# Performance work log

Hardware: AMD Instinct MI355X
Metric: run time of the kernel (lower is better)

The kernel has to match this reference:

```python
import jax, jax.numpy as jnp
import numpy as np

N = 100000   # num nodes
E = 2000000  # num edges
D = 32       # feature dim (input_dim == hidden)
L = 6        # num layers
R = 50       # num relations
B = 64       # num query source nodes
EPS = 1e-6


def setup_inputs() -> dict:
    key = jax.random.key(0)
    ks = jax.random.split(key, 7)
    edge_index = jax.random.randint(ks[0], (E, 2), 0, N)
    edge_type = jax.random.randint(ks[1], (E,), 0, R)
    edge_weight = jnp.ones((E,), jnp.float32)
    h_index = jax.random.randint(ks[2], (B,), 0, N)
    rel_emb = jax.random.normal(ks[3], (L, R, D), jnp.float32) * 0.1
    W = jax.random.normal(ks[4], (L, 13 * D, D), jnp.float32) * (1.0 / np.sqrt(13 * D))
    b = jnp.zeros((L, D), jnp.float32)
    return dict(edge_index=edge_index, edge_type=edge_type, edge_weight=edge_weight,
                h_index=h_index, rel_emb=rel_emb, W=W, b=b)


def _layer(x, boundary, node_in, node_out, edge_type, edge_weight, rel, W, b, degree_out):
    # message: distmult  (E, D)
    msg = x[node_in] * rel[edge_type]
    # append boundary as self-loop messages -> (E+N, D)
    msg = jnp.concatenate([msg, boundary], axis=0)
    seg = jnp.concatenate([node_out, jnp.arange(N)], axis=0)
    w = jnp.concatenate([edge_weight, jnp.ones((N,), x.dtype)], axis=0)[:, None]
    mw = msg * w
    cnt = jax.ops.segment_sum(jnp.ones_like(w), seg, num_segments=N)  # (N,1), >=1
    mean = jax.ops.segment_sum(mw, seg, num_segments=N) / cnt
    sq_mean = jax.ops.segment_sum((msg * msg) * w, seg, num_segments=N) / cnt
    mx = jax.ops.segment_max(mw, seg, num_segments=N)
    mn = jax.ops.segment_min(mw, seg, num_segments=N)
    std = jnp.sqrt(jnp.clip(sq_mean - mean * mean, EPS, None))
    # interleave per-channel [mean, max, min, std] -> (N, 4D)
    feat = jnp.stack([mean, mx, mn, std], axis=-1).reshape(N, 4 * D)
    scale = jnp.log(degree_out)              # (N, 1)
    scale = scale / scale.mean()
    scales = jnp.concatenate([jnp.ones_like(scale), scale,
                              1.0 / jnp.clip(scale, 1e-2, None)], axis=-1)  # (N, 3)
    update = (feat[:, :, None] * scales[:, None, :]).reshape(N, 12 * D)
    out = jnp.concatenate([x, update], axis=-1) @ W + b  # (N, D)
    return jax.nn.relu(out)


def reference(edge_index, edge_type, edge_weight, h_index, rel_emb, W, b):
    node_in = edge_index[:, 0]
    node_out = edge_index[:, 1]
    boundary = jnp.zeros((N, D), jnp.float32).at[h_index].set(1.0)
    degree_out = (jax.ops.segment_sum(edge_weight, node_out, num_segments=N) + 1.0)[:, None]
    x = boundary
    for i in range(L):
        x = _layer(x, boundary, node_in, node_out, edge_type, edge_weight,
                   rel_emb[i], W[i], b[i], degree_out)
    return x  # node_feature (N, D)
```

## Files before the change

### kernel.cpp

```cpp
#include <hip/hip_runtime.h>
#include <math.h>

#define NN 100000
#define EE 2000000
#define DD 32
#define LL 6
#define RR 50
#define BB 64
#define SCAN_BLK 98


typedef __attribute__((ext_vector_type(8))) short bf16x8;
typedef __attribute__((ext_vector_type(4))) float f32x4;

__device__ __forceinline__ unsigned short f2bf(float f) {
    unsigned int u = __float_as_uint(f);
    u = (u + 0x7FFFu + ((u >> 16) & 1u)) >> 16;
    return (unsigned short)u;
}
__device__ __forceinline__ float bf2f(unsigned short h) {
    return __uint_as_float((unsigned int)h << 16);
}

__global__ void hist_kernel(const int* __restrict__ ei, int* __restrict__ cnt) {
    for (int e = blockIdx.x * blockDim.x + threadIdx.x; e < EE; e += gridDim.x * blockDim.x)
        atomicAdd(&cnt[ei[2 * e + 1]], 1);
}

__global__ void boundary_kernel(const int* __restrict__ h, float* __restrict__ bnd,
                                float* __restrict__ x0, unsigned short* __restrict__ xbf0) {
    int t = blockIdx.x * blockDim.x + threadIdx.x;
    if (t >= BB * DD) return;
    int bidx = t >> 5, d = t & 31;
    int node = h[bidx];
    x0[node * DD + d] = 1.0f;
    if (xbf0) xbf0[node * DD + d] = 0x3F80;
    if (d == 0) bnd[node] = 1.0f;
}

__global__ void scanA_kernel(const int* __restrict__ cnt, int* __restrict__ rowptr,
                             int* __restrict__ bsum) {
    __shared__ int sh[1024];
    const int idx = blockIdx.x * 1024 + threadIdx.x;
    const int v = (idx < NN) ? cnt[idx] : 0;
    sh[threadIdx.x] = v;
    __syncthreads();
    for (int off = 1; off < 1024; off <<= 1) {
        int t = (threadIdx.x >= (unsigned)off) ? sh[threadIdx.x - off] : 0;
        __syncthreads();
        sh[threadIdx.x] += t;
        __syncthreads();
    }
    if (idx < NN) rowptr[idx] = sh[threadIdx.x] - v;
    if (threadIdx.x == 1023) bsum[blockIdx.x] = sh[1023];
}

__global__ void scanB_kernel(const int* __restrict__ bsum, int* __restrict__ boff,
                             int* __restrict__ rowptr) {
    __shared__ int sh[128];
    const int t = threadIdx.x;
    const int v = (t < SCAN_BLK) ? bsum[t] : 0;
    sh[t] = v;
    __syncthreads();
    for (int off = 1; off < 128; off <<= 1) {
        int u = (t >= off) ? sh[t - off] : 0;
        __syncthreads();
        sh[t] += u;
        __syncthreads();
    }
    if (t < SCAN_BLK) boff[t] = sh[t] - v;
    if (t == SCAN_BLK - 1) rowptr[NN] = sh[t];
}

__global__ void scanC_kernel(int* __restrict__ rowptr, int* __restrict__ cursor,
                             const int* __restrict__ boff) {
    const int idx = blockIdx.x * 1024 + threadIdx.x;
    if (idx < NN) {
        const int r = rowptr[idx] + boff[blockIdx.x];
        rowptr[idx] = r;
        cursor[idx] = r;
    }
}

__global__ void logsum_kernel(const int* __restrict__ cnt, double* __restrict__ out) {
    __shared__ double sh[256];
    double local = 0.0;
    for (int i = blockIdx.x * blockDim.x + threadIdx.x; i < NN; i += gridDim.x * blockDim.x)
        local += log((double)cnt[i] + 1.0);
    sh[threadIdx.x] = local;
    __syncthreads();
    for (int o = 128; o > 0; o >>= 1) {
        if (threadIdx.x < (unsigned)o) sh[threadIdx.x] += sh[threadIdx.x + o];
        __syncthreads();
    }
    if (threadIdx.x == 0) atomicAdd(out, sh[0]);
}

__global__ void scalefin_kernel(const int* __restrict__ cnt, const double* __restrict__ logsum,
                                float* __restrict__ scalev, float* __restrict__ iscalev) {
    float mean = (float)(logsum[0] / (double)NN);
    for (int i = blockIdx.x * blockDim.x + threadIdx.x; i < NN; i += gridDim.x * blockDim.x) {
        float s = logf((float)cnt[i] + 1.0f) / mean;
        scalev[i] = s;
        iscalev[i] = 1.0f / fmaxf(s, 0.01f);
    }
}

__global__ void scatterX_kernel(const int* __restrict__ ei, const int* __restrict__ et,
                                int* __restrict__ cursor, int* __restrict__ recs) {
    const int slice = blockIdx.x & 7;
    const int sb = blockIdx.x >> 3;
    const int nsb = gridDim.x >> 3;
    const int lo = slice * (NN / 8);
    const int hi = (slice == 7) ? NN : lo + (NN / 8);
    const int2* ei2 = (const int2*)ei;
    for (int e = sb * blockDim.x + threadIdx.x; e < EE; e += nsb * blockDim.x) {
        const int2 p = ei2[e];
        if (p.y >= lo && p.y < hi) {
            const int pos = atomicAdd(&cursor[p.y], 1);
            recs[pos] = (p.x << 6) | et[e];
        }
    }
}

__global__ __launch_bounds__(256, 4) void aggbf_kernel(
    const unsigned short* __restrict__ xbf, float* __restrict__ feat,
    const int* __restrict__ recs, const int* __restrict__ rowptr,
    const float* __restrict__ bnd, const float* __restrict__ rel_l) {
    __shared__ float rel_s[RR * 32];
    {
        const float4* r4 = (const float4*)rel_l;
        float4* rs4 = (float4*)rel_s;
        for (int i = threadIdx.x; i < (RR * 32) / 4; i += 256) rs4[i] = r4[i];
    }
    __syncthreads();

    const int lane = threadIdx.x & 63;
    const int half = lane >> 5;
    const int d = lane & 31;
    const int wid = blockIdx.x * 4 + (threadIdx.x >> 6);
    const int nwaves = gridDim.x * 4;

    for (int n0 = wid * 2; n0 < NN; n0 += nwaves * 2) {
        const int nA = n0, nB = n0 + 1;
        const int rowA = rowptr[nA], endA = rowptr[nA + 1];
        const int rowB = rowptr[nB], endB = rowptr[nB + 1];
        const float bvA = bnd[nA], bvB = bnd[nB];

        float sA = (half == 0) ? bvA : 0.f, qA = sA;
        float mxA = bvA, mnA = bvA;
        float sB = (half == 0) ? bvB : 0.f, qB = sB;
        float mxB = bvB, mnB = bvB;

        int eA = rowA + half, eB = rowB + half;

#define ACC_A(M) { sA += (M); qA = fmaf((M), (M), qA); mxA = fmaxf(mxA, (M)); mnA = fminf(mnA, (M)); }
#define ACC_B(M) { sB += (M); qB = fmaf((M), (M), qB); mxB = fmaxf(mxB, (M)); mnB = fminf(mnB, (M)); }
#define MSG(P) (bf2f(xbf[((P) >> 6) * DD + d]) * rel_s[((P) & 63) * DD + d])

        while (eA + 6 < endA && eB + 6 < endB) {
            const int pa0 = recs[eA], pa1 = recs[eA + 2], pa2 = recs[eA + 4], pa3 = recs[eA + 6];
            const int pb0 = recs[eB], pb1 = recs[eB + 2], pb2 = recs[eB + 4], pb3 = recs[eB + 6];
            const float ma0 = MSG(pa0), ma1 = MSG(pa1), ma2 = MSG(pa2), ma3 = MSG(pa3);
            const float mb0 = MSG(pb0), mb1 = MSG(pb1), mb2 = MSG(pb2), mb3 = MSG(pb3);
            ACC_A(ma0); ACC_A(ma1); ACC_A(ma2); ACC_A(ma3);
            ACC_B(mb0); ACC_B(mb1); ACC_B(mb2); ACC_B(mb3);
            eA += 8; eB += 8;
        }
        while (eA + 2 < endA) {
            const int pa0 = recs[eA], pa1 = recs[eA + 2];
            const float ma0 = MSG(pa0), ma1 = MSG(pa1);
            ACC_A(ma0); ACC_A(ma1);
            eA += 4;
        }
        while (eB + 2 < endB) {
            const int pb0 = recs[eB], pb1 = recs[eB + 2];
            const float mb0 = MSG(pb0), mb1 = MSG(pb1);
            ACC_B(mb0); ACC_B(mb1);
            eB += 4;
        }
        if (eA < endA) { const float m0 = MSG(recs[eA]); ACC_A(m0); }
        if (eB < endB) { const float m0 = MSG(recs[eB]); ACC_B(m0); }
#undef MSG
#undef ACC_A
#undef ACC_B

        sA += __shfl_xor(sA, 32); qA += __shfl_xor(qA, 32);
        mxA = fmaxf(mxA, __shfl_xor(mxA, 32)); mnA = fminf(mnA, __shfl_xor(mnA, 32));
        sB += __shfl_xor(sB, 32); qB += __shfl_xor(qB, 32);
        mxB = fmaxf(mxB, __shfl_xor(mxB, 32)); mnB = fminf(mnB, __shfl_xor(mnB, 32));

        const float invA = 1.0f / (float)(endA - rowA + 1);
        const float invB = 1.0f / (float)(endB - rowB + 1);
        if (half == 0) {
            const float mean = sA * invA;
            const float stdv = sqrtf(fmaxf(qA * invA - mean * mean, 1e-6f));
            float* fb = feat + (size_t)nA * 128;
            fb[d] = mean; fb[32 + d] = mxA; fb[64 + d] = mnA; fb[96 + d] = stdv;
        } else {
            const float mean = sB * invB;
            const float stdv = sqrtf(fmaxf(qB * invB - mean * mean, 1e-6f));
            float* fb = feat + (size_t)nB * 128;
            fb[d] = mean; fb[32 + d] = mxB; fb[64 + d] = mnB; fb[96 + d] = stdv;
        }
    }
}

__global__ __launch_bounds__(256, 4) void agg_kernel(
    const float* __restrict__ xin, float* __restrict__ feat,
    const int* __restrict__ recs, const int* __restrict__ rowptr,
    const float* __restrict__ bnd, const float* __restrict__ rel_l) {
    __shared__ float rel_s[RR * 32];
    {
        const float4* r4 = (const float4*)rel_l;
        float4* rs4 = (float4*)rel_s;
        for (int i = threadIdx.x; i < (RR * 32) / 4; i += 256) rs4[i] = r4[i];
    }
    __syncthreads();

    const int lane = threadIdx.x & 63;
    const int half = lane >> 5;
    const int d = lane & 31;
    const int wid = blockIdx.x * 4 + (threadIdx.x >> 6);
    const int nwaves = gridDim.x * 4;

    for (int n0 = wid * 2; n0 < NN; n0 += nwaves * 2) {
        const int nA = n0, nB = n0 + 1;
        const int rowA = rowptr[nA], endA = rowptr[nA + 1];
        const int rowB = rowptr[nB], endB = rowptr[nB + 1];
        const float bvA = bnd[nA], bvB = bnd[nB];

        float sA = (half == 0) ? bvA : 0.f, qA = sA;
        float mxA = bvA, mnA = bvA;
        float sB = (half == 0) ? bvB : 0.f, qB = sB;
        float mxB = bvB, mnB = bvB;

        int eA = rowA + half, eB = rowB + half;
#define STEP_A { const int p0_ = recs[eA]; const int p1_ = recs[eA + 2];                  \
        const float m0_ = xin[(p0_ >> 6) * DD + d] * rel_s[(p0_ & 63) * DD + d];           \
        const float m1_ = xin[(p1_ >> 6) * DD + d] * rel_s[(p1_ & 63) * DD + d];           \
        sA += m0_; qA = fmaf(m0_, m0_, qA); mxA = fmaxf(mxA, m0_); mnA = fminf(mnA, m0_);  \
        sA += m1_; qA = fmaf(m1_, m1_, qA); mxA = fmaxf(mxA, m1_); mnA = fminf(mnA, m1_);  \
        eA += 4; }
#define STEP_B { const int p0_ = recs[eB]; const int p1_ = recs[eB + 2];                  \
        const float m0_ = xin[(p0_ >> 6) * DD + d] * rel_s[(p0_ & 63) * DD + d];           \
        const float m1_ = xin[(p1_ >> 6) * DD + d] * rel_s[(p1_ & 63) * DD + d];           \
        sB += m0_; qB = fmaf(m0_, m0_, qB); mxB = fmaxf(mxB, m0_); mnB = fminf(mnB, m0_);  \
        sB += m1_; qB = fmaf(m1_, m1_, qB); mxB = fmaxf(mxB, m1_); mnB = fminf(mnB, m1_);  \
        eB += 4; }
        while (eA + 2 < endA && eB + 2 < endB) { STEP_A; STEP_B; }
        while (eA + 2 < endA) { STEP_A; }
        while (eB + 2 < endB) { STEP_B; }
#undef STEP_A
#undef STEP_B
        if (eA < endA) {
            const int p0_ = recs[eA];
            const float m0_ = xin[(p0_ >> 6) * DD + d] * rel_s[(p0_ & 63) * DD + d];
            sA += m0_; qA = fmaf(m0_, m0_, qA); mxA = fmaxf(mxA, m0_); mnA = fminf(mnA, m0_);
        }
        if (eB < endB) {
            const int p0_ = recs[eB];
            const float m0_ = xin[(p0_ >> 6) * DD + d] * rel_s[(p0_ & 63) * DD + d];
            sB += m0_; qB = fmaf(m0_, m0_, qB); mxB = fmaxf(mxB, m0_); mnB = fminf(mnB, m0_);
        }

        sA += __shfl_xor(sA, 32); qA += __shfl_xor(qA, 32);
        mxA = fmaxf(mxA, __shfl_xor(mxA, 32)); mnA = fminf(mnA, __shfl_xor(mnA, 32));
        sB += __shfl_xor(sB, 32); qB += __shfl_xor(qB, 32);
        mxB = fmaxf(mxB, __shfl_xor(mxB, 32)); mnB = fminf(mnB, __shfl_xor(mnB, 32));

        const float invA = 1.0f / (float)(endA - rowA + 1);
        const float invB = 1.0f / (float)(endB - rowB + 1);
        if (half == 0) {
            const float mean = sA * invA;
            const float stdv = sqrtf(fmaxf(qA * invA - mean * mean, 1e-6f));
            float* fb = feat + (size_t)nA * 128;
            fb[d] = mean; fb[32 + d] = mxA; fb[64 + d] = mnA; fb[96 + d] = stdv;
        } else {
            const float mean = sB * invB;
            const float stdv = sqrtf(fmaxf(qB * invB - mean * mean, 1e-6f));
            float* fb = feat + (size_t)nB * 128;
            fb[d] = mean; fb[32 + d] = mxB; fb[64 + d] = mnB; fb[96 + d] = stdv;
        }
    }
}

__global__ __launch_bounds__(256, 2) void epmm_kernel(
    const float* __restrict__ xin, const float* __restrict__ feat,
    float* __restrict__ xout, unsigned short* __restrict__ xbf_out,
    const float* __restrict__ scalev, const float* __restrict__ iscalev,
    const float* __restrict__ Wl, const float* __restrict__ bl) {
    __shared__ unsigned short Wf[13 * 2 * 64 * 8];
    __shared__ unsigned short off_sel[416];
    __shared__ float b_s[32];
    __shared__ unsigned short stage[4][16 * 161];

    for (int idx = threadIdx.x; idx < 13 * 2 * 64 * 8; idx += 256) {
        const int i = idx & 7, l = (idx >> 3) & 63, h = (idx >> 9) & 1, kk = idx >> 10;
        const int k = kk * 32 + (l >> 4) * 8 + i;
        const int col = h * 16 + (l & 15);
        Wf[idx] = f2bf(Wl[k * 32 + col]);
    }
    for (int k = threadIdx.x; k < 416; k += 256) {
        unsigned short os;
        if (k < 32) os = (unsigned short)k;
        else {
            const int d = (k - 32) / 12, r = (k - 32) % 12, kf = r / 3, s = r % 3;
            os = (unsigned short)((32 + kf * 32 + d) | (s << 8));
        }
        off_sel[k] = os;
    }
    if (threadIdx.x < 32) b_s[threadIdx.x] = bl[threadIdx.x];
    __syncthreads();

    const int lane = threadIdx.x & 63;
    const int wslot = threadIdx.x >> 6;
    const int wid = blockIdx.x * 4 + wslot;
    const int nwaves = gridDim.x * 4;
    unsigned short* stg = &stage[wslot][0];
    const int arow = lane & 15;
    const int kg = lane >> 4;
    const int ccol = lane & 15;

    for (int tile = wid; tile < NN / 16; tile += nwaves) {
        const int base = tile * 16;
        for (int idx = lane; idx < 512; idx += 64) {
            const int rr = idx >> 5, c = idx & 31;
            stg[rr * 161 + c] = f2bf(xin[(base + rr) * DD + c]);
        }
        for (int idx = lane; idx < 2048; idx += 64) {
            const int rr = idx >> 7, c = idx & 127;
            stg[rr * 161 + 32 + c] = f2bf(feat[(size_t)(base + rr) * 128 + c]);
        }
        const float sclR = scalev[base + arow], isclR = iscalev[base + arow];
        const unsigned short* srow = &stg[arow * 161];

        f32x4 acc0 = {0.f, 0.f, 0.f, 0.f}, acc1 = {0.f, 0.f, 0.f, 0.f};
#pragma unroll
        for (int kk = 0; kk < 13; kk++) {
            bf16x8 a;
#pragma unroll
            for (int i = 0; i < 8; i++) {
                const int k = kk * 32 + kg * 8 + i;
                const unsigned short os = off_sel[k];
                const int off = os & 255;
                const int s = os >> 8;
                float v = bf2f(srow[off]);
                v = (s == 0) ? v : (s == 1 ? v * sclR : v * isclR);
                a[i] = (short)f2bf(v);
            }
            const bf16x8 b0 = *(const bf16x8*)&Wf[((kk * 2 + 0) * 64 + lane) * 8];
            const bf16x8 b1 = *(const bf16x8*)&Wf[((kk * 2 + 1) * 64 + lane) * 8];
            acc0 = __builtin_amdgcn_mfma_f32_16x16x32_bf16(a, b0, acc0, 0, 0, 0);
            acc1 = __builtin_amdgcn_mfma_f32_16x16x32_bf16(a, b1, acc1, 0, 0, 0);
        }
#pragma unroll
        for (int r = 0; r < 4; r++) {
            const int orow = base + kg * 4 + r;
            const float v0 = fmaxf(acc0[r] + b_s[ccol], 0.0f);
            const float v1 = fmaxf(acc1[r] + b_s[ccol + 16], 0.0f);
            xout[orow * DD + ccol] = v0;
            xout[orow * DD + ccol + 16] = v1;
            if (xbf_out) {
                xbf_out[orow * DD + ccol] = f2bf(v0);
                xbf_out[orow * DD + ccol + 16] = f2bf(v1);
            }
        }
    }
}

__global__ __launch_bounds__(512, 2) void fused_kernel(
    const float* __restrict__ xin, float* __restrict__ xout,
    const int* __restrict__ recs, const int* __restrict__ rowptr,
    const float* __restrict__ bnd, const float* __restrict__ scalev,
    const float* __restrict__ iscalev,
    const float* __restrict__ Wl, const float* __restrict__ bl,
    const float* __restrict__ rel_l) {
    __shared__ float W_s[416 * 32];
    __shared__ float rel_s[RR * 32];
    __shared__ float b_s[32];
    {
        const float4* w4 = (const float4*)Wl;
        float4* ws4 = (float4*)W_s;
        for (int i = threadIdx.x; i < (416 * 32) / 4; i += 512) ws4[i] = w4[i];
        const float4* r4 = (const float4*)rel_l;
        float4* rs4 = (float4*)rel_s;
        for (int i = threadIdx.x; i < (RR * 32) / 4; i += 512) rs4[i] = r4[i];
        if (threadIdx.x < 32) b_s[threadIdx.x] = bl[threadIdx.x];
    }
    __syncthreads();

    const int lane = threadIdx.x & 63;
    const int half = lane >> 5;
    const int d = lane & 31;
    const int wid = blockIdx.x * 8 + (threadIdx.x >> 6);
    const int nwaves = gridDim.x * 8;

    for (int n0 = wid * 2; n0 < NN; n0 += nwaves * 2) {
        const int nA = n0, nB = n0 + 1;
        const int rowA = rowptr[nA], endA = rowptr[nA + 1];
        const int rowB = rowptr[nB], endB = rowptr[nB + 1];
        const float bvA = bnd[nA], bvB = bnd[nB];
        const float sclA = scalev[nA], isclA = iscalev[nA];
        const float sclB = scalev[nB], isclB = iscalev[nB];
        const float xvA = xin[nA * DD + d], xvB = xin[nB * DD + d];

        float sA = (half == 0) ? bvA : 0.f, qA = sA;
        float mxA = bvA, mnA = bvA;
        float sB = (half == 0) ? bvB : 0.f, qB = sB;
        float mxB = bvB, mnB = bvB;

        int eA = rowA + half, eB = rowB + half;
#define STEP_A { const int p0_ = recs[eA]; const int p1_ = recs[eA + 2];                  \
        const float m0_ = xin[(p0_ >> 6) * DD + d] * rel_s[(p0_ & 63) * DD + d];           \
        const float m1_ = xin[(p1_ >> 6) * DD + d] * rel_s[(p1_ & 63) * DD + d];           \
        sA += m0_; qA = fmaf(m0_, m0_, qA); mxA = fmaxf(mxA, m0_); mnA = fminf(mnA, m0_);  \
        sA += m1_; qA = fmaf(m1_, m1_, qA); mxA = fmaxf(mxA, m1_); mnA = fminf(mnA, m1_);  \
        eA += 4; }
#define STEP_B { const int p0_ = recs[eB]; const int p1_ = recs[eB + 2];                  \
        const float m0_ = xin[(p0_ >> 6) * DD + d] * rel_s[(p0_ & 63) * DD + d];           \
        const float m1_ = xin[(p1_ >> 6) * DD + d] * rel_s[(p1_ & 63) * DD + d];           \
        sB += m0_; qB = fmaf(m0_, m0_, qB); mxB = fmaxf(mxB, m0_); mnB = fminf(mnB, m0_);  \
        sB += m1_; qB = fmaf(m1_, m1_, qB); mxB = fmaxf(mxB, m1_); mnB = fminf(mnB, m1_);  \
        eB += 4; }
        while (eA + 2 < endA && eB + 2 < endB) { STEP_A; STEP_B; }
        while (eA + 2 < endA) { STEP_A; }
        while (eB + 2 < endB) { STEP_B; }
#undef STEP_A
#undef STEP_B
        if (eA < endA) {
            const int p0_ = recs[eA];
            const float m0_ = xin[(p0_ >> 6) * DD + d] * rel_s[(p0_ & 63) * DD + d];
            sA += m0_; qA = fmaf(m0_, m0_, qA); mxA = fmaxf(mxA, m0_); mnA = fminf(mnA, m0_);
        }
        if (eB < endB) {
            const int p0_ = recs[eB];
            const float m0_ = xin[(p0_ >> 6) * DD + d] * rel_s[(p0_ & 63) * DD + d];
            sB += m0_; qB = fmaf(m0_, m0_, qB); mxB = fmaxf(mxB, m0_); mnB = fminf(mnB, m0_);
        }

        sA += __shfl_xor(sA, 32); qA += __shfl_xor(qA, 32);
        mxA = fmaxf(mxA, __shfl_xor(mxA, 32)); mnA = fminf(mnA, __shfl_xor(mnA, 32));
        sB += __shfl_xor(sB, 32); qB += __shfl_xor(qB, 32);
        mxB = fmaxf(mxB, __shfl_xor(mxB, 32)); mnB = fminf(mnB, __shfl_xor(mnB, 32));

        const float invA = 1.0f / (float)(endA - rowA + 1);
        const float invB = 1.0f / (float)(endB - rowB + 1);
        const float meanA = sA * invA;
        const float stdA = sqrtf(fmaxf(qA * invA - meanA * meanA, 1e-6f));
        const float meanB = sB * invB;
        const float stdB = sqrtf(fmaxf(qB * invB - meanB * meanB, 1e-6f));

        float xv[2] = {xvA, xvB};
        float f0[2] = {meanA, meanB}, f1[2] = {mxA, mxB};
        float f2[2] = {mnA, mnB}, f3[2] = {stdA, stdB};
        float aX[2] = {0.f, 0.f}, aA[2] = {0.f, 0.f}, aB[2] = {0.f, 0.f}, aC[2] = {0.f, 0.f};
        const int srcBase = half * 48;
#pragma unroll
        for (int t = 0; t < 16; t++) {
            const int src = srcBase + t;
            const int i = half * 16 + t;
            const float w0 = W_s[i * 32 + d];
            const float* wr = &W_s[(32 + i * 12) * 32 + d];
            const float w1 = wr[0 * 32], w2 = wr[1 * 32], w3 = wr[2 * 32];
            const float w4 = wr[3 * 32], w5 = wr[4 * 32], w6 = wr[5 * 32];
            const float w7 = wr[6 * 32], w8 = wr[7 * 32], w9 = wr[8 * 32];
            const float wa = wr[9 * 32], wb = wr[10 * 32], wc = wr[11 * 32];
#pragma unroll
            for (int p = 0; p < 2; p++) {
                const float xb = __shfl(xv[p], src);
                const float g0 = __shfl(f0[p], src);
                const float g1 = __shfl(f1[p], src);
                const float g2 = __shfl(f2[p], src);
                const float g3 = __shfl(f3[p], src);
                aX[p] = fmaf(xb, w0, aX[p]);
                aA[p] = fmaf(g0, w1, aA[p]); aB[p] = fmaf(g0, w2, aB[p]); aC[p] = fmaf(g0, w3, aC[p]);
                aA[p] = fmaf(g1, w4, aA[p]); aB[p] = fmaf(g1, w5, aB[p]); aC[p] = fmaf(g1, w6, aC[p]);
                aA[p] = fmaf(g2, w7, aA[p]); aB[p] = fmaf(g2, w8, aB[p]); aC[p] = fmaf(g2, w9, aC[p]);
                aA[p] = fmaf(g3, wa, aA[p]); aB[p] = fmaf(g3, wb, aB[p]); aC[p] = fmaf(g3, wc, aC[p]);
            }
        }
        float rA = aX[0] + aA[0] + sclA * aB[0] + isclA * aC[0];
        float rB = aX[1] + aA[1] + sclB * aB[1] + isclB * aC[1];
        rA += __shfl_xor(rA, 32);
        rB += __shfl_xor(rB, 32);
        rA = fmaxf(rA + b_s[d], 0.0f);
        rB = fmaxf(rB + b_s[d], 0.0f);
        if (half == 0) {
            xout[nA * DD + d] = rA;
            xout[nB * DD + d] = rB;
        }
    }
}

extern "C" void kernel_launch(void* const* d_in, const int* in_sizes, int n_in,
                              void* d_out, int out_size, void* d_ws, size_t ws_size,
                              hipStream_t stream) {
    const int* ei = (const int*)d_in[0];
    const int* et = (const int*)d_in[1];
    const int* hidx = (const int*)d_in[3];
    const float* rel = (const float*)d_in[4];
    const float* W = (const float*)d_in[5];
    const float* b = (const float*)d_in[6];

    char* ws = (char*)d_ws;
    int* cnt = (int*)(ws + 0);
    int* rowptr = (int*)(ws + 400000);
    int* cursor = (int*)(ws + 800016);
    float* scalev = (float*)(ws + 1200016);
    float* iscalev = (float*)(ws + 1600016);
    float* bnd = (float*)(ws + 2000016);
    double* logsum = (double*)(ws + 2400016);
    int* bsum = (int*)(ws + 2400032);
    int* boff = (int*)(ws + 2400544);
    int* recs = (int*)(ws + 2401056);

    const bool bf = (ws_size >= (size_t)100001088);
    const bool split = bf || (ws_size >= (size_t)87201088);
    float* feat = (float*)(ws + 10401088);
    float* xbuf0 = split ? (float*)(ws + 61601088) : (float*)(ws + 10401088);
    float* xbuf1 = split ? (float*)(ws + 74401088) : (float*)(ws + 23201088);
    unsigned short* xbf0 = bf ? (unsigned short*)(ws + 87201088) : nullptr;
    unsigned short* xbf1 = bf ? (unsigned short*)(ws + 93601088) : nullptr;

    hipMemsetAsync(ws, 0, 2400032, stream);
    hipMemsetAsync(recs + EE, 0, 8 * sizeof(int), stream);
    hipMemsetAsync(xbuf0, 0, NN * DD * sizeof(float), stream);
    if (bf) hipMemsetAsync(xbf0, 0, NN * DD * sizeof(unsigned short), stream);

    hist_kernel<<<1024, 256, 0, stream>>>(ei, cnt);
    boundary_kernel<<<(BB * DD + 255) / 256, 256, 0, stream>>>(hidx, bnd, xbuf0, xbf0);
    scanA_kernel<<<SCAN_BLK, 1024, 0, stream>>>(cnt, rowptr, bsum);
    scanB_kernel<<<1, 128, 0, stream>>>(bsum, boff, rowptr);
    scanC_kernel<<<SCAN_BLK, 1024, 0, stream>>>(rowptr, cursor, boff);
    logsum_kernel<<<256, 256, 0, stream>>>(cnt, logsum);
    scalefin_kernel<<<400, 256, 0, stream>>>(cnt, logsum, scalev, iscalev);
    scatterX_kernel<<<1024, 256, 0, stream>>>(ei, et, cursor, recs);

    float* xout_final = (float*)d_out;
    for (int l = 0; l < LL; l++) {
        const float* xin = (l % 2 == 0) ? xbuf0 : xbuf1;
        float* xout = (l == LL - 1) ? xout_final : ((l % 2 == 0) ? xbuf1 : xbuf0);
        const float* Wl = W + (size_t)l * 416 * 32;
        const float* bl = b + (size_t)l * 32;
        const float* rl = rel + (size_t)l * RR * 32;
        if (bf) {
            unsigned short* xbf_in = (l % 2 == 0) ? xbf0 : xbf1;
            unsigned short* xbf_out = (l == LL - 1) ? nullptr : ((l % 2 == 0) ? xbf1 : xbf0);
            aggbf_kernel<<<2048, 256, 0, stream>>>(xbf_in, feat, recs, rowptr, bnd, rl);
            epmm_kernel<<<1024, 256, 0, stream>>>(xin, feat, xout, xbf_out, scalev, iscalev, Wl, bl);
        } else if (split) {
            agg_kernel<<<2048, 256, 0, stream>>>(xin, feat, recs, rowptr, bnd, rl);
            epmm_kernel<<<1024, 256, 0, stream>>>(xin, feat, xout, nullptr, scalev, iscalev, Wl, bl);
        } else {
            fused_kernel<<<512, 512, 0, stream>>>(
                xin, xout, recs, rowptr, bnd, scalev, iscalev, Wl, bl, rl);
        }
    }
}
```

Measured before the change: 801.5 us.

## Store aggregated features in bf16 and prescale MFMA operand rows in epmm

The aggregation kernel now writes its mean/max/min/std features as bf16 instead of fp32, which halves the intermediate feature traffic. The epilogue GEMM reads the bf16 layer input and features, expands the three degree scalings once into a staged 416-wide bf16 row, and feeds MFMA directly, so the per-element lookup-table decode in the inner loop is gone. fp32 node buffers are dropped except for the final output, the workspace requirement is lower, and the unused agg path is removed. The cost is an extra bf16 rounding of the features, and launch bounds and grid size are changed.

New measurement: 708.3 us. 1.13x faster.

```diff
diff --git a/kernel.cpp b/kernel.cpp
--- a/kernel.cpp
+++ b/kernel.cpp
@@ -33,7 +33,7 @@
     if (t >= BB * DD) return;
     int bidx = t >> 5, d = t & 31;
     int node = h[bidx];
-    x0[node * DD + d] = 1.0f;
+    if (x0) x0[node * DD + d] = 1.0f;
     if (xbf0) xbf0[node * DD + d] = 0x3F80;
     if (d == 0) bnd[node] = 1.0f;
 }
@@ -124,7 +124,7 @@
 }
 
 __global__ __launch_bounds__(256, 4) void aggbf_kernel(
-    const unsigned short* __restrict__ xbf, float* __restrict__ feat,
+    const unsigned short* __restrict__ xbf, unsigned short* __restrict__ featb,
     const int* __restrict__ recs, const int* __restrict__ rowptr,
     const float* __restrict__ bnd, const float* __restrict__ rel_l) {
     __shared__ float rel_s[RR * 32];
@@ -195,40 +195,130 @@
         if (half == 0) {
             const float mean = sA * invA;
             const float stdv = sqrtf(fmaxf(qA * invA - mean * mean, 1e-6f));
-            float* fb = feat + (size_t)nA * 128;
-            fb[d] = mean; fb[32 + d] = mxA; fb[64 + d] = mnA; fb[96 + d] = stdv;
+            unsigned short* fb = featb + (size_t)nA * 128;
+            fb[d] = f2bf(mean); fb[32 + d] = f2bf(mxA);
+            fb[64 + d] = f2bf(mnA); fb[96 + d] = f2bf(stdv);
         } else {
             const float mean = sB * invB;
             const float stdv = sqrtf(fmaxf(qB * invB - mean * mean, 1e-6f));
-            float* fb = feat + (size_t)nB * 128;
-            fb[d] = mean; fb[32 + d] = mxB; fb[64 + d] = mnB; fb[96 + d] = stdv;
-        }
-    }
-}
-
-__global__ __launch_bounds__(256, 4) void agg_kernel(
-    const float* __restrict__ xin, float* __restrict__ feat,
+            unsigned short* fb = featb + (size_t)nB * 128;
+            fb[d] = f2bf(mean); fb[32 + d] = f2bf(mxB);
+            fb[64 + d] = f2bf(mnB); fb[96 + d] = f2bf(stdv);
+        }
+    }
+}
+
+__global__ __launch_bounds__(256, 1) void epmm_kernel(
+    const unsigned short* __restrict__ xbf_in, const unsigned short* __restrict__ featb,
+    unsigned short* __restrict__ xbf_out, float* __restrict__ fout,
+    const float* __restrict__ scalev, const float* __restrict__ iscalev,
+    const float* __restrict__ Wl, const float* __restrict__ bl) {
+    __shared__ unsigned short Wf[13 * 2 * 64 * 8];
+    __shared__ float b_s[32];
+    __shared__ unsigned short stage[4][16 * 424];
+
+    for (int idx = threadIdx.x; idx < 13 * 2 * 64 * 8; idx += 256) {
+        const int i = idx & 7, l = (idx >> 3) & 63, h = (idx >> 9) & 1, kk = idx >> 10;
+        const int k = kk * 32 + (l >> 4) * 8 + i;
+        const int col = h * 16 + (l & 15);
+        Wf[idx] = f2bf(Wl[k * 32 + col]);
+    }
+    if (threadIdx.x < 32) b_s[threadIdx.x] = bl[threadIdx.x];
+    __syncthreads();
+
+    const int lane = threadIdx.x & 63;
+    const int wslot = threadIdx.x >> 6;
+    const int wid = blockIdx.x * 4 + wslot;
+    const int nwaves = gridDim.x * 4;
+    unsigned short* stg = &stage[wslot][0];
+    const int d = lane & 31;
+    const int hi = lane >> 5;
+    const int arow = lane & 15;
+    const int kg = lane >> 4;
+    const int ccol = lane & 15;
+
+    for (int tile = wid; tile < NN / 16; tile += nwaves) {
+        const int base = tile * 16;
+#pragma unroll
+        for (int rr = 0; rr < 8; rr++) {
+            const int r = hi * 8 + rr;
+            stg[r * 424 + d] = xbf_in[(base + r) * DD + d];
+        }
+        for (int r = 0; r < 16; r++) {
+            const float sclR = scalev[base + r];
+            const float isclR = iscalev[base + r];
+#pragma unroll
+            for (int kq = 0; kq < 2; kq++) {
+                const int kf = hi * 2 + kq;
+                const float f = bf2f(featb[(size_t)(base + r) * 128 + kf * 32 + d]);
+                unsigned short* w = &stg[r * 424 + 32 + d * 12 + kf * 3];
+                w[0] = f2bf(f);
+                w[1] = f2bf(f * sclR);
+                w[2] = f2bf(f * isclR);
+            }
+        }
+        const unsigned short* srow = &stg[arow * 424];
+        f32x4 acc0 = {0.f, 0.f, 0.f, 0.f}, acc1 = {0.f, 0.f, 0.f, 0.f};
+#pragma unroll
+        for (int kk = 0; kk < 13; kk++) {
+            const bf16x8 a = *(const bf16x8*)&srow[kk * 32 + kg * 8];
+            const bf16x8 b0 = *(const bf16x8*)&Wf[((kk * 2 + 0) * 64 + lane) * 8];
+            const bf16x8 b1 = *(const bf16x8*)&Wf[((kk * 2 + 1) * 64 + lane) * 8];
+            acc0 = __builtin_amdgcn_mfma_f32_16x16x32_bf16(a, b0, acc0, 0, 0, 0);
+            acc1 = __builtin_amdgcn_mfma_f32_16x16x32_bf16(a, b1, acc1, 0, 0, 0);
+        }
+#pragma unroll
+        for (int r = 0; r < 4; r++) {
+            const int orow = base + kg * 4 + r;
+            const float v0 = fmaxf(acc0[r] + b_s[ccol], 0.0f);
+            const float v1 = fmaxf(acc1[r] + b_s[ccol + 16], 0.0f);
+            if (xbf_out) {
+                xbf_out[orow * DD + ccol] = f2bf(v0);
+                xbf_out[orow * DD + ccol + 16] = f2bf(v1);
+            }
+            if (fout) {
+                fout[orow * DD + ccol] = v0;
+                fout[orow * DD + ccol + 16] = v1;
+            }
+        }
+    }
+}
+
+__global__ __launch_bounds__(512, 2) void fused_kernel(
+    const float* __restrict__ xin, float* __restrict__ xout,
     const int* __restrict__ recs, const int* __restrict__ rowptr,
-    const float* __restrict__ bnd, const float* __restrict__ rel_l) {
+    const float* __restrict__ bnd, const float* __restrict__ scalev,
+    const float* __restrict__ iscalev,
+    const float* __restrict__ Wl, const float* __restrict__ bl,
+    const float* __restrict__ rel_l) {
+    __shared__ float W_s[416 * 32];
     __shared__ float rel_s[RR * 32];
+    __shared__ float b_s[32];
     {
+        const float4* w4 = (const float4*)Wl;
+        float4* ws4 = (float4*)W_s;
+        for (int i = threadIdx.x; i < (416 * 32) / 4; i += 512) ws4[i] = w4[i];
         const float4* r4 = (const float4*)rel_l;
         float4* rs4 = (float4*)rel_s;
-        for (int i = threadIdx.x; i < (RR * 32) / 4; i += 256) rs4[i] = r4[i];
+        for (int i = threadIdx.x; i < (RR * 32) / 4; i += 512) rs4[i] = r4[i];
+        if (threadIdx.x < 32) b_s[threadIdx.x] = bl[threadIdx.x];
     }
     __syncthreads();
 
     const int lane = threadIdx.x & 63;
     const int half = lane >> 5;
     const int d = lane & 31;
-    const int wid = blockIdx.x * 4 + (threadIdx.x >> 6);
-    const int nwaves = gridDim.x * 4;
+    const int wid = blockIdx.x * 8 + (threadIdx.x >> 6);
+    const int nwaves = gridDim.x * 8;
 
     for (int n0 = wid * 2; n0 < NN; n0 += nwaves * 2) {
         const int nA = n0, nB = n0 + 1;
         const int rowA = rowptr[nA], endA = rowptr[nA + 1];
         const int rowB = rowptr[nB], endB = rowptr[nB + 1];
         const float bvA = bnd[nA], bvB = bnd[nB];
+        const float sclA = scalev[nA], isclA = iscalev[nA];
+        const float sclB = scalev[nB], isclB = iscalev[nB];
+        const float xvA = xin[nA * DD + d], xvB = xin[nB * DD + d];
 
         float sA = (half == 0) ? bvA : 0.f, qA = sA;
         float mxA = bvA, mnA = bvA;
@@ -271,181 +361,6 @@
 
         const float invA = 1.0f / (float)(endA - rowA + 1);
         const float invB = 1.0f / (float)(endB - rowB + 1);
-        if (half == 0) {
-            const float mean = sA * invA;
-            const float stdv = sqrtf(fmaxf(qA * invA - mean * mean, 1e-6f));
-            float* fb = feat + (size_t)nA * 128;
-            fb[d] = mean; fb[32 + d] = mxA; fb[64 + d] = mnA; fb[96 + d] = stdv;
-        } else {
-            const float mean = sB * invB;
-            const float stdv = sqrtf(fmaxf(qB * invB - mean * mean, 1e-6f));
-            float* fb = feat + (size_t)nB * 128;
-            fb[d] = mean; fb[32 + d] = mxB; fb[64 + d] = mnB; fb[96 + d] = stdv;
-        }
-    }
-}
-
-__global__ __launch_bounds__(256, 2) void epmm_kernel(
-    const float* __restrict__ xin, const float* __restrict__ feat,
-    float* __restrict__ xout, unsigned short* __restrict__ xbf_out,
-    const float* __restrict__ scalev, const float* __restrict__ iscalev,
-    const float* __restrict__ Wl, const float* __restrict__ bl) {
-    __shared__ unsigned short Wf[13 * 2 * 64 * 8];
-    __shared__ unsigned short off_sel[416];
-    __shared__ float b_s[32];
-    __shared__ unsigned short stage[4][16 * 161];
-
-    for (int idx = threadIdx.x; idx < 13 * 2 * 64 * 8; idx += 256) {
-        const int i = idx & 7, l = (idx >> 3) & 63, h = (idx >> 9) & 1, kk = idx >> 10;
-        const int k = kk * 32 + (l >> 4) * 8 + i;
-        const int col = h * 16 + (l & 15);
-        Wf[idx] = f2bf(Wl[k * 32 + col]);
-    }
-    for (int k = threadIdx.x; k < 416; k += 256) {
-        unsigned short os;
-        if (k < 32) os = (unsigned short)k;
-        else {
-            const int d = (k - 32) / 12, r = (k - 32) % 12, kf = r / 3, s = r % 3;
-            os = (unsigned short)((32 + kf * 32 + d) | (s << 8));
-        }
-        off_sel[k] = os;
-    }
-    if (threadIdx.x < 32) b_s[threadIdx.x] = bl[threadIdx.x];
-    __syncthreads();
-
-    const int lane = threadIdx.x & 63;
-    const int wslot = threadIdx.x >> 6;
-    const int wid = blockIdx.x * 4 + wslot;
-    const int nwaves = gridDim.x * 4;
-    unsigned short* stg = &stage[wslot][0];
-    const int arow = lane & 15;
-    const int kg = lane >> 4;
-    const int ccol = lane & 15;
-
-    for (int tile = wid; tile < NN / 16; tile += nwaves) {
-        const int base = tile * 16;
-        for (int idx = lane; idx < 512; idx += 64) {
-            const int rr = idx >> 5, c = idx & 31;
-            stg[rr * 161 + c] = f2bf(xin[(base + rr) * DD + c]);
-        }
-        for (int idx = lane; idx < 2048; idx += 64) {
-            const int rr = idx >> 7, c = idx & 127;
-            stg[rr * 161 + 32 + c] = f2bf(feat[(size_t)(base + rr) * 128 + c]);
-        }
-        const float sclR = scalev[base + arow], isclR = iscalev[base + arow];
-        const unsigned short* srow = &stg[arow * 161];
-
-        f32x4 acc0 = {0.f, 0.f, 0.f, 0.f}, acc1 = {0.f, 0.f, 0.f, 0.f};
-#pragma unroll
-        for (int kk = 0; kk < 13; kk++) {
-            bf16x8 a;
-#pragma unroll
-            for (int i = 0; i < 8; i++) {
-                const int k = kk * 32 + kg * 8 + i;
-                const unsigned short os = off_sel[k];
-                const int off = os & 255;
-                const int s = os >> 8;
-                float v = bf2f(srow[off]);
-                v = (s == 0) ? v : (s == 1 ? v * sclR : v * isclR);
-                a[i] = (short)f2bf(v);
-            }
-            const bf16x8 b0 = *(const bf16x8*)&Wf[((kk * 2 + 0) * 64 + lane) * 8];
-            const bf16x8 b1 = *(const bf16x8*)&Wf[((kk * 2 + 1) * 64 + lane) * 8];
-            acc0 = __builtin_amdgcn_mfma_f32_16x16x32_bf16(a, b0, acc0, 0, 0, 0);
-            acc1 = __builtin_amdgcn_mfma_f32_16x16x32_bf16(a, b1, acc1, 0, 0, 0);
-        }
-#pragma unroll
-        for (int r = 0; r < 4; r++) {
-            const int orow = base + kg * 4 + r;
-            const float v0 = fmaxf(acc0[r] + b_s[ccol], 0.0f);
-            const float v1 = fmaxf(acc1[r] + b_s[ccol + 16], 0.0f);
-            xout[orow * DD + ccol] = v0;
-            xout[orow * DD + ccol + 16] = v1;
-            if (xbf_out) {
-                xbf_out[orow * DD + ccol] = f2bf(v0);
-                xbf_out[orow * DD + ccol + 16] = f2bf(v1);
-            }
-        }
-    }
-}
-
-__global__ __launch_bounds__(512, 2) void fused_kernel(
-    const float* __restrict__ xin, float* __restrict__ xout,
-    const int* __restrict__ recs, const int* __restrict__ rowptr,
-    const float* __restrict__ bnd, const float* __restrict__ scalev,
-    const float* __restrict__ iscalev,
-    const float* __restrict__ Wl, const float* __restrict__ bl,
-    const float* __restrict__ rel_l) {
-    __shared__ float W_s[416 * 32];
-    __shared__ float rel_s[RR * 32];
-    __shared__ float b_s[32];
-    {
-        const float4* w4 = (const float4*)Wl;
-        float4* ws4 = (float4*)W_s;
-        for (int i = threadIdx.x; i < (416 * 32) / 4; i += 512) ws4[i] = w4[i];
-        const float4* r4 = (const float4*)rel_l;
-        float4* rs4 = (float4*)rel_s;
-        for (int i = threadIdx.x; i < (RR * 32) / 4; i += 512) rs4[i] = r4[i];
-        if (threadIdx.x < 32) b_s[threadIdx.x] = bl[threadIdx.x];
-    }
-    __syncthreads();
-
-    const int lane = threadIdx.x & 63;
-    const int half = lane >> 5;
-    const int d = lane & 31;
-    const int wid = blockIdx.x * 8 + (threadIdx.x >> 6);
-    const int nwaves = gridDim.x * 8;
-
-    for (int n0 = wid * 2; n0 < NN; n0 += nwaves * 2) {
-        const int nA = n0, nB = n0 + 1;
-        const int rowA = rowptr[nA], endA = rowptr[nA + 1];
-        const int rowB = rowptr[nB], endB = rowptr[nB + 1];
-        const float bvA = bnd[nA], bvB = bnd[nB];
-        const float sclA = scalev[nA], isclA = iscalev[nA];
-        const float sclB = scalev[nB], isclB = iscalev[nB];
-        const float xvA = xin[nA * DD + d], xvB = xin[nB * DD + d];
-
-        float sA = (half == 0) ? bvA : 0.f, qA = sA;
-        float mxA = bvA, mnA = bvA;
-        float sB = (half == 0) ? bvB : 0.f, qB = sB;
-        float mxB = bvB, mnB = bvB;
-
-        int eA = rowA + half, eB = rowB + half;
-#define STEP_A { const int p0_ = recs[eA]; const int p1_ = recs[eA + 2];                  \
-        const float m0_ = xin[(p0_ >> 6) * DD + d] * rel_s[(p0_ & 63) * DD + d];           \
-        const float m1_ = xin[(p1_ >> 6) * DD + d] * rel_s[(p1_ & 63) * DD + d];           \
-        sA += m0_; qA = fmaf(m0_, m0_, qA); mxA = fmaxf(mxA, m0_); mnA = fminf(mnA, m0_);  \
-        sA += m1_; qA = fmaf(m1_, m1_, qA); mxA = fmaxf(mxA, m1_); mnA = fminf(mnA, m1_);  \
-        eA += 4; }
-#define STEP_B { const int p0_ = recs[eB]; const int p1_ = recs[eB + 2];                  \
-        const float m0_ = xin[(p0_ >> 6) * DD + d] * rel_s[(p0_ & 63) * DD + d];           \
-        const float m1_ = xin[(p1_ >> 6) * DD + d] * rel_s[(p1_ & 63) * DD + d];           \
-        sB += m0_; qB = fmaf(m0_, m0_, qB); mxB = fmaxf(mxB, m0_); mnB = fminf(mnB, m0_);  \
-        sB += m1_; qB = fmaf(m1_, m1_, qB); mxB = fmaxf(mxB, m1_); mnB = fminf(mnB, m1_);  \
-        eB += 4; }
-        while (eA + 2 < endA && eB + 2 < endB) { STEP_A; STEP_B; }
-        while (eA + 2 < endA) { STEP_A; }
-        while (eB + 2 < endB) { STEP_B; }
-#undef STEP_A
-#undef STEP_B
-        if (eA < endA) {
-            const int p0_ = recs[eA];
-            const float m0_ = xin[(p0_ >> 6) * DD + d] * rel_s[(p0_ & 63) * DD + d];
-            sA += m0_; qA = fmaf(m0_, m0_, qA); mxA = fmaxf(mxA, m0_); mnA = fminf(mnA, m0_);
-        }
-        if (eB < endB) {
-            const int p0_ = recs[eB];
-            const float m0_ = xin[(p0_ >> 6) * DD + d] * rel_s[(p0_ & 63) * DD + d];
-            sB += m0_; qB = fmaf(m0_, m0_, qB); mxB = fmaxf(mxB, m0_); mnB = fminf(mnB, m0_);
-        }
-
-        sA += __shfl_xor(sA, 32); qA += __shfl_xor(qA, 32);
-        mxA = fmaxf(mxA, __shfl_xor(mxA, 32)); mnA = fminf(mnA, __shfl_xor(mnA, 32));
-        sB += __shfl_xor(sB, 32); qB += __shfl_xor(qB, 32);
-        mxB = fmaxf(mxB, __shfl_xor(mxB, 32)); mnB = fminf(mnB, __shfl_xor(mnB, 32));
-
-        const float invA = 1.0f / (float)(endA - rowA + 1);
-        const float invB = 1.0f / (float)(endB - rowB + 1);
         const float meanA = sA * invA;
         const float stdA = sqrtf(fmaxf(qA * invA - meanA * meanA, 1e-6f));
         const float meanB = sB * invB;
@@ -515,21 +430,21 @@
     int* boff = (int*)(ws + 2400544);
     int* recs = (int*)(ws + 2401056);
 
-    const bool bf = (ws_size >= (size_t)100001088);
-    const bool split = bf || (ws_size >= (size_t)87201088);
-    float* feat = (float*)(ws + 10401088);
-    float* xbuf0 = split ? (float*)(ws + 61601088) : (float*)(ws + 10401088);
-    float* xbuf1 = split ? (float*)(ws + 74401088) : (float*)(ws + 23201088);
-    unsigned short* xbf0 = bf ? (unsigned short*)(ws + 87201088) : nullptr;
-    unsigned short* xbf1 = bf ? (unsigned short*)(ws + 93601088) : nullptr;
+    const bool bf = (ws_size >= (size_t)48801088);
+    unsigned short* featb = (unsigned short*)(ws + 10401088);
+    unsigned short* xbf0 = (unsigned short*)(ws + 36001088);
+    unsigned short* xbf1 = (unsigned short*)(ws + 42401088);
+    float* xbuf0 = (float*)(ws + 10401088);
+    float* xbuf1 = (float*)(ws + 23201088);
 
     hipMemsetAsync(ws, 0, 2400032, stream);
     hipMemsetAsync(recs + EE, 0, 8 * sizeof(int), stream);
-    hipMemsetAsync(xbuf0, 0, NN * DD * sizeof(float), stream);
     if (bf) hipMemsetAsync(xbf0, 0, NN * DD * sizeof(unsigned short), stream);
+    else hipMemsetAsync(xbuf0, 0, NN * DD * sizeof(float), stream);
 
     hist_kernel<<<1024, 256, 0, stream>>>(ei, cnt);
-    boundary_kernel<<<(BB * DD + 255) / 256, 256, 0, stream>>>(hidx, bnd, xbuf0, xbf0);
+    boundary_kernel<<<(BB * DD + 255) / 256, 256, 0, stream>>>(
+        hidx, bnd, bf ? nullptr : xbuf0, bf ? xbf0 : nullptr);
     scanA_kernel<<<SCAN_BLK, 1024, 0, stream>>>(cnt, rowptr, bsum);
     scanB_kernel<<<1, 128, 0, stream>>>(bsum, boff, rowptr);
     scanC_kernel<<<SCAN_BLK, 1024, 0, stream>>>(rowptr, cursor, boff);
@@ -539,20 +454,19 @@
 
     float* xout_final = (float*)d_out;
     for (int l = 0; l < LL; l++) {
-        const float* xin = (l % 2 == 0) ? xbuf0 : xbuf1;
-        float* xout = (l == LL - 1) ? xout_final : ((l % 2 == 0) ? xbuf1 : xbuf0);
         const float* Wl = W + (size_t)l * 416 * 32;
         const float* bl = b + (size_t)l * 32;
         const float* rl = rel + (size_t)l * RR * 32;
         if (bf) {
             unsigned short* xbf_in = (l % 2 == 0) ? xbf0 : xbf1;
             unsigned short* xbf_out = (l == LL - 1) ? nullptr : ((l % 2 == 0) ? xbf1 : xbf0);
-            aggbf_kernel<<<2048, 256, 0, stream>>>(xbf_in, feat, recs, rowptr, bnd, rl);
-            epmm_kernel<<<1024, 256, 0, stream>>>(xin, feat, xout, xbf_out, scalev, iscalev, Wl, bl);
-        } else if (split) {
-            agg_kernel<<<2048, 256, 0, stream>>>(xin, feat, recs, rowptr, bnd, rl);
-            epmm_kernel<<<1024, 256, 0, stream>>>(xin, feat, xout, nullptr, scalev, iscalev, Wl, bl);
+            float* fout = (l == LL - 1) ? xout_final : nullptr;
+            aggbf_kernel<<<2048, 256, 0, stream>>>(xbf_in, featb, recs, rowptr, bnd, rl);
+            epmm_kernel<<<1536, 256, 0, stream>>>(xbf_in, featb, xbf_out, fout,
+                                                  scalev, iscalev, Wl, bl);
         } else {
+            const float* xin = (l % 2 == 0) ? xbuf0 : xbuf1;
+            float* xout = (l == LL - 1) ? xout_final : ((l % 2 == 0) ? xbuf1 : xbuf0);
             fused_kernel<<<512, 512, 0, stream>>>(
                 xin, xout, recs, rowptr, bnd, scalev, iscalev, Wl, bl, rl);
         }
```
